# Kernel optimization log

Measured on AMD Instinct MI355X. Metric: run time of the kernel, lower is better.

## Reference

```python
import jax, jax.numpy as jnp
import numpy as np

B, S, E, D = 8, 2048, 1024, 512

def setup_inputs() -> dict:
    key = jax.random.key(0)
    ks = jax.random.split(key, 7)
    scale = 1.0 / np.sqrt(E)
    return {
        "X": jax.random.normal(ks[0], (B, S, E), dtype=jnp.float32),
        "lam": jnp.float32(0.8),
        "W_q": jax.random.uniform(ks[1], (E, 2 * D), jnp.float32, -scale, scale),
        "b_q": jax.random.uniform(ks[2], (2 * D,), jnp.float32, -scale, scale),
        "W_k": jax.random.uniform(ks[3], (E, 2 * D), jnp.float32, -scale, scale),
        "b_k": jax.random.uniform(ks[4], (2 * D,), jnp.float32, -scale, scale),
        "W_v": jax.random.uniform(ks[5], (E, D), jnp.float32, -scale, scale),
        "b_v": jax.random.uniform(ks[6], (D,), jnp.float32, -scale, scale),
    }

def reference(X, lam, W_q, b_q, W_k, b_k, W_v, b_v):
    # Projections
    Q = X @ W_q + b_q          # [B, S, 2D]
    K = X @ W_k + b_k          # [B, S, 2D]
    V = X @ W_v + b_v          # [B, S, D]
    Q1, Q2 = Q[..., :D], Q[..., D:]
    K1, K2 = K[..., :D], K[..., D:]
    s = 1.0 / np.sqrt(D)
    A1 = jnp.einsum('bqd,bkd->bqk', Q1, K1) * s  # [B, S, S]
    A2 = jnp.einsum('bqd,bkd->bqk', Q2, K2) * s
    P = jax.nn.softmax(A1, axis=-1) - lam * jax.nn.softmax(A2, axis=-1)
    return jnp.einsum('bqk,bkd->bqd', P, V)      # [B, S, D]
```

## Files before the change

### kernel.cpp

```cpp
#include <hip/hip_runtime.h>


typedef unsigned short u16;
typedef short    bf16x8 __attribute__((ext_vector_type(8)));
typedef unsigned short u16x8 __attribute__((ext_vector_type(8)));
typedef unsigned short u16x4 __attribute__((ext_vector_type(4)));
typedef float    f32x4  __attribute__((ext_vector_type(4)));

typedef __attribute__((address_space(3))) unsigned int       lds_uint;
typedef __attribute__((address_space(1))) const unsigned int gl_uint;

__device__ __forceinline__ void glds16(const void* g, void* l) {
  __builtin_amdgcn_global_load_lds((gl_uint*)g, (lds_uint*)l, 16, 0, 0);
}

__device__ __forceinline__ u16 to_bf16(float f) {
  unsigned u = __float_as_uint(f);
  return (u16)((u + 0x7FFFu + ((u >> 16) & 1u)) >> 16);
}
__device__ __forceinline__ float b2f(u16 h) {
  return __uint_as_float(((unsigned)h) << 16);
}


__global__ void cvt_x(const float4* __restrict__ in, u16x4* __restrict__ out, int n4) {
  int i = blockIdx.x * 256 + threadIdx.x;
  if (i >= n4) return;
  float4 v = in[i];
  u16x4 o;
  o[0] = to_bf16(v.x); o[1] = to_bf16(v.y); o[2] = to_bf16(v.z); o[3] = to_bf16(v.w);
  out[i] = o;
}

__global__ void transpose_cvt(const float* __restrict__ in, u16* __restrict__ out,
                              int R, int C) {
  __shared__ float t[64][65];
  int c0 = blockIdx.x * 64, r0 = blockIdx.y * 64;
  int tx = threadIdx.x, ty = threadIdx.y;
  #pragma unroll
  for (int i = 0; i < 64; i += 4)
    t[ty + i][tx] = in[(long)(r0 + ty + i) * C + c0 + tx];
  __syncthreads();
  #pragma unroll
  for (int i = 0; i < 64; i += 4)
    out[(long)(c0 + ty + i) * R + r0 + tx] = to_bf16(t[tx][ty + i]);
}

__global__ void concat2(const float* __restrict__ a, const float* __restrict__ b,
                        float* __restrict__ o, int n) {
  int i = blockIdx.x * 256 + threadIdx.x;
  if (i < n) o[i] = a[i];
  else if (i < 2 * n) o[i] = b[i - n];
}

__device__ __forceinline__ void swizzle_tiles(int& tm, int& tn) {
  int nx = gridDim.x;
  int lin = blockIdx.y * nx + blockIdx.x;
  int span = nx * 4;
  int group = lin / span;
  int ing = lin % span;
  tm = group * 4 + (ing & 3);
  tn = ing >> 2;
}

__global__ __launch_bounds__(256, 4) void gemm_nt(
    const u16* __restrict__ A, int lda,
    const u16* __restrict__ B, int ldb,
    u16* __restrict__ C1, u16* __restrict__ C2, int splitN, int ldc,
    int Kd, float scale,
    const float* __restrict__ bias, int biasMode)
{
  __shared__ u16 SM[2][8192];
  u16* As = SM[0];
  u16* Bs = SM[1];

  int tid = threadIdx.x;
  int wave = tid >> 6, lane = tid & 63;
  int quad = lane >> 4, ln = lane & 15;
  int wm = wave >> 1, wn = wave & 1;
  int tm, tn;
  swizzle_tiles(tm, tn);
  int c8 = lane >> 3, ml = lane & 7;

  const f32x4 fz = {0.f, 0.f, 0.f, 0.f};
  f32x4 acc[4][4];
  #pragma unroll
  for (int i = 0; i < 4; i++)
    #pragma unroll
    for (int j = 0; j < 4; j++) acc[i][j] = fz;

  const u16* Abase = A + (long)(tm * 128 + ml) * lda + c8 * 8;
  const u16* Bbase = B + (long)(tn * 128 + ml) * ldb + c8 * 8;

  for (int kt = 0; kt < Kd; kt += 64) {
    __syncthreads();
    #pragma unroll
    for (int i = 0; i < 4; i++) {
      int mg = wave * 4 + i;
      glds16(Abase + (long)mg * 8 * lda + kt, &As[mg * 512]);
      glds16(Bbase + (long)mg * 8 * ldb + kt, &Bs[mg * 512]);
    }
    __syncthreads();
    #pragma unroll
    for (int ks = 0; ks < 2; ks++) {
      bf16x8 af[4], bfr[4];
      int c = ks * 4 + quad;
      #pragma unroll
      for (int mt = 0; mt < 4; mt++) {
        int m = wm * 64 + mt * 16 + ln;
        af[mt] = *(const bf16x8*)&As[((m >> 3) * 64 + c * 8 + (m & 7)) * 8];
      }
      #pragma unroll
      for (int nt = 0; nt < 4; nt++) {
        int n = wn * 64 + nt * 16 + ln;
        bfr[nt] = *(const bf16x8*)&Bs[((n >> 3) * 64 + c * 8 + (n & 7)) * 8];
      }
      #pragma unroll
      for (int mt = 0; mt < 4; mt++)
        #pragma unroll
        for (int nt = 0; nt < 4; nt++)
          acc[mt][nt] = __builtin_amdgcn_mfma_f32_16x16x32_bf16(af[mt], bfr[nt], acc[mt][nt], 0, 0, 0);
    }
  }

  int rowBase = tm * 128 + wm * 64;
  int colBase = tn * 128 + wn * 64;
  u16* Cw = C1; int outCol = colBase;
  if (colBase >= splitN) { Cw = C2; outCol = colBase - splitN; }
  u16* eb = &SM[0][0] + wave * 4096;

  __syncthreads();
  #pragma unroll
  for (int mt = 0; mt < 4; mt++) {
    #pragma unroll
    for (int nt = 0; nt < 4; nt++) {
      int colL = nt * 16 + ln;
      float bcol = (biasMode == 1) ? bias[colBase + colL] : 0.f;
      #pragma unroll
      for (int r = 0; r < 4; r++) {
        int rowL = mt * 16 + quad * 4 + r;
        float brow = (biasMode == 2) ? bias[rowBase + rowL] : 0.f;
        float v = acc[mt][nt][r] * scale + bcol + brow;
        eb[rowL * 64 + (((colL >> 3) ^ (rowL & 7)) << 3) + (colL & 7)] = to_bf16(v);
      }
    }
  }
  {
    int row = lane;
    long gr = (long)(rowBase + row) * ldc + outCol;
    #pragma unroll
    for (int c = 0; c < 8; c++) {
      u16x8 ch = *(const u16x8*)&eb[row * 64 + ((c ^ (row & 7)) << 3)];
      *(u16x8*)&Cw[gr + c * 8] = ch;
    }
  }
}

__device__ __forceinline__ void gemm256_core(
    const u16* __restrict__ A, int lda,
    const u16* __restrict__ B, int ldb,
    int NT, int tm, int tn, u16* SMp, f32x4 (&acc)[8][4])
{
  int tid = threadIdx.x;
  int wave = tid >> 6, lane = tid & 63;
  int quad = lane >> 4, ln = lane & 15;
  int wm = wave >> 2, wn = wave & 3;
  int c8 = lane >> 3, ml = lane & 7;

  const f32x4 fz = {0.f, 0.f, 0.f, 0.f};
  #pragma unroll
  for (int i = 0; i < 8; i++)
    #pragma unroll
    for (int j = 0; j < 4; j++) acc[i][j] = fz;

  const u16* Ab = A + (long)(tm * 256 + ml) * lda + c8 * 8;
  const u16* Bb = B + (long)(tn * 256 + ml) * ldb + c8 * 8;

  #pragma unroll
  for (int h = 0; h < 2; h++) {
    int hg = h * 16 + wave * 2;
    glds16(Ab + (long)(hg * 8) * lda,       SMp + hg * 512);
    glds16(Ab + (long)(hg * 8 + 8) * lda,   SMp + (hg + 1) * 512);
  }
  #pragma unroll
  for (int h = 0; h < 2; h++) {
    int hg = h * 16 + wave * 2;
    glds16(Bb + (long)(hg * 8) * ldb,       SMp + 2 * 16384 + hg * 512);
    glds16(Bb + (long)(hg * 8 + 8) * ldb,   SMp + 2 * 16384 + (hg + 1) * 512);
  }
  {
    int kt1 = (NT > 1) ? 64 : 0;
    #pragma unroll
    for (int h = 0; h < 2; h++) {
      int hg = h * 16 + wave * 2;
      glds16(Bb + (long)(hg * 8) * ldb + kt1,     SMp + 3 * 16384 + hg * 512);
      glds16(Bb + (long)(hg * 8 + 8) * ldb + kt1, SMp + 3 * 16384 + (hg + 1) * 512);
    }
  }
  asm volatile("s_waitcnt vmcnt(4)" ::: "memory");
  __builtin_amdgcn_s_barrier();
  __builtin_amdgcn_sched_barrier(0);

  for (int t = 0; t < NT; t++) {
    const int p = t & 1;
    const u16* Ar = SMp + p * 16384;
    const u16* Br = SMp + (2 + p) * 16384;
    bf16x8 bfr[2][4];

    #pragma unroll
    for (int q = 0; q < 4; q++) {
      bf16x8 af[2][2];
      #pragma unroll
      for (int dm = 0; dm < 2; dm++) {
        int m = wm * 128 + (q * 2 + dm) * 16 + ln;
        #pragma unroll
        for (int ks = 0; ks < 2; ks++)
          af[dm][ks] = *(const bf16x8*)(Ar + ((m >> 3) * 64 + (ks * 4 + quad) * 8 + (m & 7)) * 8);
      }
      if (q == 0) {
        #pragma unroll
        for (int nt = 0; nt < 4; nt++) {
          int n = wn * 64 + nt * 16 + ln;
          #pragma unroll
          for (int ks = 0; ks < 2; ks++)
            bfr[ks][nt] = *(const bf16x8*)(Br + ((n >> 3) * 64 + (ks * 4 + quad) * 8 + (n & 7)) * 8);
        }
      }
      if (q < 2) {
        int ktA = ((t + 1 < NT) ? (t + 1) : (NT - 1)) << 6;
        int hg = q * 16 + wave * 2;
        u16* dst = SMp + ((t + 1) & 1) * 16384;
        glds16(Ab + (long)(hg * 8) * lda + ktA,     dst + hg * 512);
        glds16(Ab + (long)(hg * 8 + 8) * lda + ktA, dst + (hg + 1) * 512);
      } else {
        int ktB = ((t + 2 < NT) ? (t + 2) : (NT - 1)) << 6;
        int hg = (q - 2) * 16 + wave * 2;
        u16* dst = SMp + (2 + p) * 16384;
        glds16(Bb + (long)(hg * 8) * ldb + ktB,     dst + hg * 512);
        glds16(Bb + (long)(hg * 8 + 8) * ldb + ktB, dst + (hg + 1) * 512);
      }
      __builtin_amdgcn_sched_barrier(0);
      __builtin_amdgcn_s_barrier();
      asm volatile("s_waitcnt lgkmcnt(0)" ::: "memory");
      __builtin_amdgcn_sched_barrier(0);
      __builtin_amdgcn_s_setprio(1);
      #pragma unroll
      for (int ks = 0; ks < 2; ks++)
        #pragma unroll
        for (int dm = 0; dm < 2; dm++)
          #pragma unroll
          for (int nt = 0; nt < 4; nt++)
            acc[q * 2 + dm][nt] = __builtin_amdgcn_mfma_f32_16x16x32_bf16(
                af[dm][ks], bfr[ks][nt], acc[q * 2 + dm][nt], 0, 0, 0);
      __builtin_amdgcn_s_setprio(0);
      __builtin_amdgcn_sched_barrier(0);
      if (q == 3) asm volatile("s_waitcnt vmcnt(4)" ::: "memory");
      __builtin_amdgcn_s_barrier();
      __builtin_amdgcn_sched_barrier(0);
    }
  }
}

__global__ __launch_bounds__(512, 2) void gemm_nt256(
    const u16* __restrict__ A, int lda,
    const u16* __restrict__ B, int ldb,
    u16* __restrict__ C1, u16* __restrict__ C2, int splitN, int ldc,
    int Kd, float scale,
    const float* __restrict__ bias, int biasMode)
{
  __shared__ u16 SM[4][16384];
  int tm, tn;
  swizzle_tiles(tm, tn);
  f32x4 acc[8][4];
  gemm256_core(A, lda, B, ldb, Kd >> 6, tm, tn, &SM[0][0], acc);

  int tid = threadIdx.x;
  int wave = tid >> 6, lane = tid & 63;
  int quad = lane >> 4, ln = lane & 15;
  int wm = wave >> 2, wn = wave & 3;

  int rowBase = tm * 256 + wm * 128;
  int colBase = tn * 256 + wn * 64;
  u16* Cw = C1; int outCol = colBase;
  if (colBase >= splitN) { Cw = C2; outCol = colBase - splitN; }
  u16* eb = &SM[0][0] + wave * 8192;

  asm volatile("s_waitcnt vmcnt(0)" ::: "memory");
  __builtin_amdgcn_s_barrier();
  __builtin_amdgcn_sched_barrier(0);

  #pragma unroll
  for (int mt = 0; mt < 8; mt++) {
    #pragma unroll
    for (int nt = 0; nt < 4; nt++) {
      int colL = nt * 16 + ln;
      float bcol = (biasMode == 1) ? bias[colBase + colL] : 0.f;
      #pragma unroll
      for (int r = 0; r < 4; r++) {
        int rowL = mt * 16 + quad * 4 + r;
        float brow = (biasMode == 2) ? bias[rowBase + rowL] : 0.f;
        float v = acc[mt][nt][r] * scale + bcol + brow;
        eb[rowL * 64 + (((colL >> 3) ^ (rowL & 7)) << 3) + (colL & 7)] = to_bf16(v);
      }
    }
  }
  #pragma unroll
  for (int rr = 0; rr < 2; rr++) {
    int row = rr * 64 + lane;
    long gr = (long)(rowBase + row) * ldc + outCol;
    #pragma unroll
    for (int c = 0; c < 8; c++) {
      u16x8 ch = *(const u16x8*)&eb[row * 64 + ((c ^ (row & 7)) << 3)];
      *(u16x8*)&Cw[gr + c * 8] = ch;
    }
  }
}

__global__ __launch_bounds__(512, 2) void gemm_s256(
    const u16* __restrict__ Q, const u16* __restrict__ K,
    u16* __restrict__ E1, u16* __restrict__ E2,
    float* __restrict__ statsP, float scale)
{
  __shared__ u16 SM[4][16384];
  int bz = blockIdx.z >> 1, half = blockIdx.z & 1;
  const u16* A = Q + (long)bz * 2097152 + half * 512;
  const u16* B = K + (long)bz * 2097152 + half * 512;
  u16* Ed = (half ? E2 : E1) + (long)bz * 4194304;
  statsP += (long)blockIdx.z * 65536;

  int tm, tn;
  swizzle_tiles(tm, tn);
  f32x4 acc[8][4];
  gemm256_core(A, 1024, B, 1024, 8 , tm, tn, &SM[0][0], acc);

  int tid = threadIdx.x;
  int wave = tid >> 6, lane = tid & 63;
  int quad = lane >> 4, ln = lane & 15;
  int wm = wave >> 2, wn = wave & 3;

  int rowBase = tm * 256 + wm * 128;
  int colBase = tn * 256 + wn * 64;
  int kb = tn * 4 + wn;
  u16* eb = &SM[0][0] + wave * 8192;

  asm volatile("s_waitcnt vmcnt(0)" ::: "memory");
  __builtin_amdgcn_s_barrier();
  __builtin_amdgcn_sched_barrier(0);

  #pragma unroll
  for (int mt = 0; mt < 8; mt++) {
    #pragma unroll
    for (int nt = 0; nt < 4; nt++) {
      int colL = nt * 16 + ln;
      #pragma unroll
      for (int r = 0; r < 4; r++) {
        int rowL = mt * 16 + quad * 4 + r;
        eb[rowL * 64 + (((colL >> 3) ^ (rowL & 7)) << 3) + (colL & 7)] =
            to_bf16(__expf(acc[mt][nt][r] * scale));
      }
    }
  }
  #pragma unroll
  for (int rr = 0; rr < 2; rr++) {
    int row = rr * 64 + lane;
    u16x8 ch[8];
    #pragma unroll
    for (int c = 0; c < 8; c++)
      ch[c] = *(const u16x8*)&eb[row * 64 + ((c ^ (row & 7)) << 3)];
    u16* Ep = Ed + (long)(rowBase + row) * 2048 + colBase;
    #pragma unroll
    for (int c = 0; c < 8; c++)
      *(u16x8*)&Ep[c * 8] = ch[c];
    float L = 0.f;
    #pragma unroll
    for (int c = 0; c < 8; c++)
      #pragma unroll
      for (int j = 0; j < 8; j++) L += b2f(ch[c][j]);
    statsP[(rowBase + row) * 32 + kb] = L;
  }
}

__global__ void stats_reduce(const float* __restrict__ sp, float* __restrict__ so,
                             const float* __restrict__ lamPtr) {
  int gid = blockIdx.x * 256 + threadIdx.x;
  const float* p = sp + (long)gid * 32;
  float L = 0.f;
  #pragma unroll
  for (int kb = 0; kb < 32; kb++) L += p[kb];
  int half = (gid >> 11) & 1;
  so[gid] = (half ? lamPtr[0] : 1.0f) / L;
}

__global__ __launch_bounds__(512, 2) void apply_pv(
    const u16* __restrict__ E1, const u16* __restrict__ E2,
    const u16* __restrict__ VT, const float* __restrict__ inv,
    float* __restrict__ Out)
{
  __shared__ u16 Vs[2][32768];
  __shared__ u16 Pb[2][4096];
  __shared__ float i1s[64], i2s[64];

  const int NT = 32;
  int b = blockIdx.x & 7, qt = blockIdx.x >> 3;
  int q0 = qt * 64;
  int tid = threadIdx.x;
  int wave = tid >> 6, lane = tid & 63, quad = lane >> 4, ln = lane & 15;
  int c8 = lane >> 3, ml = lane & 7;
  int r = tid >> 3, cg8 = tid & 7;

  const u16* e1p = E1 + ((long)b * 2048 + q0 + r) * 2048 + cg8 * 8;
  const u16* e2p = E2 + ((long)b * 2048 + q0 + r) * 2048 + cg8 * 8;
  const u16* Vbase = VT + (long)b * 2048;
  int pw = (r >> 3) * 512 + cg8 * 64 + (r & 7) * 8;

  const f32x4 fz = {0.f, 0.f, 0.f, 0.f};
  f32x4 acc[4][4];
  #pragma unroll
  for (int i = 0; i < 4; i++)
    #pragma unroll
    for (int j = 0; j < 4; j++) acc[i][j] = fz;

  if (tid < 64)       i1s[tid]       = inv[(long)(b * 2 + 0) * 2048 + q0 + tid];
  else if (tid < 128) i2s[tid - 64]  = inv[(long)(b * 2 + 1) * 2048 + q0 + (tid - 64)];
  u16x8 a1 = *(const u16x8*)(e1p);
  u16x8 a2 = *(const u16x8*)(e2p);
  __builtin_amdgcn_sched_barrier(0);
  #pragma unroll
  for (int i = 0; i < 8; i++) {
    int dg = wave * 8 + i;
    glds16(Vbase + (long)(dg * 8 + ml) * 16384 + c8 * 8, &Vs[0][dg * 512]);
  }
  __builtin_amdgcn_sched_barrier(0);
  asm volatile("s_waitcnt lgkmcnt(0)" ::: "memory");
  __builtin_amdgcn_s_barrier();
  __builtin_amdgcn_sched_barrier(0);
  float i1 = i1s[r], i2 = i2s[r];
  {
    u16x8 o;
    #pragma unroll
    for (int j = 0; j < 8; j++)
      o[j] = to_bf16(b2f(a1[j]) * i1 - b2f(a2[j]) * i2);
    *(u16x8*)&Pb[0][pw] = o;
  }
  a1 = *(const u16x8*)(e1p + 64);
  a2 = *(const u16x8*)(e2p + 64);
  __builtin_amdgcn_sched_barrier(0);
  asm volatile("s_waitcnt lgkmcnt(0)" ::: "memory");
  asm volatile("s_waitcnt vmcnt(2)" ::: "memory");
  __builtin_amdgcn_sched_barrier(0);
  __builtin_amdgcn_s_barrier();
  __builtin_amdgcn_sched_barrier(0);

  for (int t = 0; t < NT; t++) {
    const int p = t & 1;
    const u16* Vr = &Vs[p][0];
    const u16* Pr = &Pb[p][0];
    u16* Vw = &Vs[p ^ 1][0];
    u16* Pw = &Pb[p ^ 1][0];
    int ktv = ((t + 1 < NT) ? (t + 1) : (NT - 1)) << 6;
    int kte = ((t + 2 < NT) ? (t + 2) : (NT - 1)) << 6;
    bf16x8 vf[2][4];

    #pragma unroll
    for (int q = 0; q < 4; q++) {
      bf16x8 pf[2];
      #pragma unroll
      for (int ks = 0; ks < 2; ks++) {
        int m = q * 16 + ln;
        pf[ks] = *(const bf16x8*)&Pr[((m >> 3) * 64 + (ks * 4 + quad) * 8 + (m & 7)) * 8];
      }
      if (q == 0) {
        #pragma unroll
        for (int ks = 0; ks < 2; ks++)
          #pragma unroll
          for (int nt = 0; nt < 4; nt++) {
            int d = wave * 64 + nt * 16 + ln;
            vf[ks][nt] = *(const bf16x8*)&Vr[((d >> 3) * 64 + (ks * 4 + quad) * 8 + (d & 7)) * 8];
          }
      }
      #pragma unroll
      for (int i = 0; i < 2; i++) {
        int dg = wave * 8 + q * 2 + i;
        glds16(Vbase + (long)(dg * 8 + ml) * 16384 + ktv + c8 * 8, Vw + dg * 512);
      }
      if (q == 3) {
        __builtin_amdgcn_sched_barrier(0);
        u16x8 o;
        #pragma unroll
        for (int j = 0; j < 8; j++)
          o[j] = to_bf16(b2f(a1[j]) * i1 - b2f(a2[j]) * i2);
        *(u16x8*)&Pw[pw] = o;
        a1 = *(const u16x8*)(e1p + kte);
        a2 = *(const u16x8*)(e2p + kte);
      }
      __builtin_amdgcn_sched_barrier(0);
      __builtin_amdgcn_s_barrier();
      asm volatile("s_waitcnt lgkmcnt(0)" ::: "memory");
      __builtin_amdgcn_sched_barrier(0);
      __builtin_amdgcn_s_setprio(1);
      #pragma unroll
      for (int ks = 0; ks < 2; ks++)
        #pragma unroll
        for (int nt = 0; nt < 4; nt++)
          acc[q][nt] = __builtin_amdgcn_mfma_f32_16x16x32_bf16(pf[ks], vf[ks][nt], acc[q][nt], 0, 0, 0);
      __builtin_amdgcn_s_setprio(0);
      __builtin_amdgcn_sched_barrier(0);
      if (q == 3) asm volatile("s_waitcnt vmcnt(2)" ::: "memory");
      __builtin_amdgcn_s_barrier();
      __builtin_amdgcn_sched_barrier(0);
    }
  }

  #pragma unroll
  for (int mt = 0; mt < 4; mt++)
    #pragma unroll
    for (int nt = 0; nt < 4; nt++)
      #pragma unroll
      for (int r2 = 0; r2 < 4; r2++)
        Out[((long)b * 2048 + q0 + mt * 16 + quad * 4 + r2) * 512 + wave * 64 + nt * 16 + ln] =
            acc[mt][nt][r2];
}


extern "C" void kernel_launch(void* const* d_in, const int* in_sizes, int n_in,
                              void* d_out, int out_size, void* d_ws, size_t ws_size,
                              hipStream_t stream)
{
  const float* X   = (const float*)d_in[0];
  const float* lam = (const float*)d_in[1];
  const float* Wq  = (const float*)d_in[2];
  const float* bq  = (const float*)d_in[3];
  const float* Wk  = (const float*)d_in[4];
  const float* bk  = (const float*)d_in[5];
  const float* Wv  = (const float*)d_in[6];
  const float* bv  = (const float*)d_in[7];
  float* Out = (float*)d_out;
  char* ws = (char*)d_ws;

  u16*  WqkT   = (u16*)(ws + 0);
  u16*  WvT    = (u16*)(ws + 4194304);
  float* bqk   = (float*)(ws + 5242880);
  u16*  Qb     = (u16*)(ws + 6291456);
  u16*  Kb     = (u16*)(ws + 39845888);
  u16*  VTb    = (u16*)(ws + 73400320);
  u16*  Xb     = (u16*)(ws + 90177536);
  u16*  E1     = (u16*)(ws + 90177536);
  u16*  E2     = (u16*)(ws + 157286400);
  float* statsP= (float*)(ws + 224395264);
  float* invD  = (float*)(ws + 228589568);

  cvt_x<<<16384, 256, 0, stream>>>((const float4*)X, (u16x4*)Xb, 4194304);
  transpose_cvt<<<dim3(16, 16), dim3(64, 4), 0, stream>>>(Wq, WqkT, 1024, 1024);
  transpose_cvt<<<dim3(16, 16), dim3(64, 4), 0, stream>>>(Wk, WqkT + 1024 * 1024, 1024, 1024);
  transpose_cvt<<<dim3(8, 16),  dim3(64, 4), 0, stream>>>(Wv, WvT, 1024, 512);
  concat2<<<8, 256, 0, stream>>>(bq, bk, bqk, 1024);

  gemm_nt256<<<dim3(8, 64), 512, 0, stream>>>(Xb, 1024, WqkT, 1024,
                                              Qb, Kb, 1024, 1024,
                                              1024, 1.0f, bqk, 1);
  gemm_nt<<<dim3(128, 4), 256, 0, stream>>>(WvT, 1024, Xb, 1024,
                                            VTb, VTb, 1 << 30, 16384,
                                            1024, 1.0f, bv, 2);

  const float s = 0.044194173824159216f;
  gemm_s256<<<dim3(8, 8, 16), 512, 0, stream>>>(Qb, Kb, E1, E2, statsP, s);

  stats_reduce<<<128, 256, 0, stream>>>(statsP, invD, lam);
  apply_pv<<<256, 512, 0, stream>>>(E1, E2, VTb, invD, Out);
}
```

Before: 475.6 us.

## Triple-buffer B tiles and drop per-subtile barriers in GEMM main loop

The shared GEMM core now uses three LDS buffers for the B operand instead of two. At the top of each k-iteration it issues all global-to-LDS loads for the next A tile and the B tile two steps ahead. It then runs the full MFMA block with a single wait and barrier per iteration, replacing the four barrier/lgkmcnt/setprio sections per iteration. The aim is to cut synchronisation overhead and let the compiler schedule LDS reads freely. The cost is LDS per block rising from 128KB to 160KB, and fewer points where prefetch traffic is interleaved with compute.

```diff
diff --git a/kernel.cpp b/kernel.cpp
--- a/kernel.cpp
+++ b/kernel.cpp
@@ -185,79 +185,81 @@
   #pragma unroll
   for (int h = 0; h < 2; h++) {
     int hg = h * 16 + wave * 2;
-    glds16(Bb + (long)(hg * 8) * ldb,       SMp + 2 * 16384 + hg * 512);
-    glds16(Bb + (long)(hg * 8 + 8) * ldb,   SMp + 2 * 16384 + (hg + 1) * 512);
+    glds16(Bb + (long)(hg * 8) * ldb,       SMp + 32768 + hg * 512);
+    glds16(Bb + (long)(hg * 8 + 8) * ldb,   SMp + 32768 + (hg + 1) * 512);
   }
   {
     int kt1 = (NT > 1) ? 64 : 0;
     #pragma unroll
     for (int h = 0; h < 2; h++) {
       int hg = h * 16 + wave * 2;
-      glds16(Bb + (long)(hg * 8) * ldb + kt1,     SMp + 3 * 16384 + hg * 512);
-      glds16(Bb + (long)(hg * 8 + 8) * ldb + kt1, SMp + 3 * 16384 + (hg + 1) * 512);
+      glds16(Bb + (long)(hg * 8) * ldb + kt1,     SMp + 49152 + hg * 512);
+      glds16(Bb + (long)(hg * 8 + 8) * ldb + kt1, SMp + 49152 + (hg + 1) * 512);
     }
   }
   asm volatile("s_waitcnt vmcnt(4)" ::: "memory");
   __builtin_amdgcn_s_barrier();
   __builtin_amdgcn_sched_barrier(0);
 
+  int bcur = 0;
   for (int t = 0; t < NT; t++) {
     const int p = t & 1;
     const u16* Ar = SMp + p * 16384;
-    const u16* Br = SMp + (2 + p) * 16384;
+    const u16* Br = SMp + 32768 + bcur * 16384;
+
+    {
+      int ktA = ((t + 1 < NT) ? (t + 1) : (NT - 1)) << 6;
+      u16* dA = SMp + ((t + 1) & 1) * 16384;
+      #pragma unroll
+      for (int h = 0; h < 2; h++) {
+        int hg = h * 16 + wave * 2;
+        glds16(Ab + (long)(hg * 8) * lda + ktA,     dA + hg * 512);
+        glds16(Ab + (long)(hg * 8 + 8) * lda + ktA, dA + (hg + 1) * 512);
+      }
+      int ktB = ((t + 2 < NT) ? (t + 2) : (NT - 1)) << 6;
+      int bst = bcur + 2; if (bst >= 3) bst -= 3;
+      u16* dB = SMp + 32768 + bst * 16384;
+      #pragma unroll
+      for (int h = 0; h < 2; h++) {
+        int hg = h * 16 + wave * 2;
+        glds16(Bb + (long)(hg * 8) * ldb + ktB,     dB + hg * 512);
+        glds16(Bb + (long)(hg * 8 + 8) * ldb + ktB, dB + (hg + 1) * 512);
+      }
+    }
+    __builtin_amdgcn_sched_barrier(0);
+
     bf16x8 bfr[2][4];
-
-    #pragma unroll
-    for (int q = 0; q < 4; q++) {
+    #pragma unroll
+    for (int nt = 0; nt < 4; nt++) {
+      int n = wn * 64 + nt * 16 + ln;
+      #pragma unroll
+      for (int ks = 0; ks < 2; ks++)
+        bfr[ks][nt] = *(const bf16x8*)(Br + ((n >> 3) * 64 + (ks * 4 + quad) * 8 + (n & 7)) * 8);
+    }
+    #pragma unroll
+    for (int g = 0; g < 4; g++) {
       bf16x8 af[2][2];
       #pragma unroll
       for (int dm = 0; dm < 2; dm++) {
-        int m = wm * 128 + (q * 2 + dm) * 16 + ln;
+        int m = wm * 128 + (g * 2 + dm) * 16 + ln;
         #pragma unroll
         for (int ks = 0; ks < 2; ks++)
           af[dm][ks] = *(const bf16x8*)(Ar + ((m >> 3) * 64 + (ks * 4 + quad) * 8 + (m & 7)) * 8);
       }
-      if (q == 0) {
-        #pragma unroll
-        for (int nt = 0; nt < 4; nt++) {
-          int n = wn * 64 + nt * 16 + ln;
-          #pragma unroll
-          for (int ks = 0; ks < 2; ks++)
-            bfr[ks][nt] = *(const bf16x8*)(Br + ((n >> 3) * 64 + (ks * 4 + quad) * 8 + (n & 7)) * 8);
-        }
-      }
-      if (q < 2) {
-        int ktA = ((t + 1 < NT) ? (t + 1) : (NT - 1)) << 6;
-        int hg = q * 16 + wave * 2;
-        u16* dst = SMp + ((t + 1) & 1) * 16384;
-        glds16(Ab + (long)(hg * 8) * lda + ktA,     dst + hg * 512);
-        glds16(Ab + (long)(hg * 8 + 8) * lda + ktA, dst + (hg + 1) * 512);
-      } else {
-        int ktB = ((t + 2 < NT) ? (t + 2) : (NT - 1)) << 6;
-        int hg = (q - 2) * 16 + wave * 2;
-        u16* dst = SMp + (2 + p) * 16384;
-        glds16(Bb + (long)(hg * 8) * ldb + ktB,     dst + hg * 512);
-        glds16(Bb + (long)(hg * 8 + 8) * ldb + ktB, dst + (hg + 1) * 512);
-      }
-      __builtin_amdgcn_sched_barrier(0);
-      __builtin_amdgcn_s_barrier();
-      asm volatile("s_waitcnt lgkmcnt(0)" ::: "memory");
-      __builtin_amdgcn_sched_barrier(0);
-      __builtin_amdgcn_s_setprio(1);
       #pragma unroll
       for (int ks = 0; ks < 2; ks++)
         #pragma unroll
         for (int dm = 0; dm < 2; dm++)
           #pragma unroll
           for (int nt = 0; nt < 4; nt++)
-            acc[q * 2 + dm][nt] = __builtin_amdgcn_mfma_f32_16x16x32_bf16(
-                af[dm][ks], bfr[ks][nt], acc[q * 2 + dm][nt], 0, 0, 0);
-      __builtin_amdgcn_s_setprio(0);
-      __builtin_amdgcn_sched_barrier(0);
-      if (q == 3) asm volatile("s_waitcnt vmcnt(4)" ::: "memory");
-      __builtin_amdgcn_s_barrier();
-      __builtin_amdgcn_sched_barrier(0);
-    }
+            acc[g * 2 + dm][nt] = __builtin_amdgcn_mfma_f32_16x16x32_bf16(
+                af[dm][ks], bfr[ks][nt], acc[g * 2 + dm][nt], 0, 0, 0);
+    }
+
+    asm volatile("s_waitcnt vmcnt(4)" ::: "memory");
+    __builtin_amdgcn_s_barrier();
+    __builtin_amdgcn_sched_barrier(0);
+    bcur = (bcur == 2) ? 0 : bcur + 1;
   }
 }
 
@@ -268,7 +270,7 @@
     int Kd, float scale,
     const float* __restrict__ bias, int biasMode)
 {
-  __shared__ u16 SM[4][16384];
+  __shared__ u16 SM[5][16384];
   int tm, tn;
   swizzle_tiles(tm, tn);
   f32x4 acc[8][4];
@@ -321,7 +323,7 @@
     u16* __restrict__ E1, u16* __restrict__ E2,
     float* __restrict__ statsP, float scale)
 {
-  __shared__ u16 SM[4][16384];
+  __shared__ u16 SM[5][16384];
   int bz = blockIdx.z >> 1, half = blockIdx.z & 1;
   const u16* A = Q + (long)bz * 2097152 + half * 512;
   const u16* B = K + (long)bz * 2097152 + half * 512;
```

After: 478.9 us. No clear change (+0.7%).

## Make QK projection and score GEMMs persistent with multi-tile continuous pipelines

Applied to the files above, without the earlier changes.

Replaces the one-tile-per-block 256x256 GEMMs with persistent 256-block kernels. Each block walks several M tiles back to back (two for the projection, four for the score GEMM) in a single continuous K-loop pipeline, and runs the epilogue inline every 16 or 8 K-steps through a small per-wave LDS staging buffer. The goal is to remove per-tile prologue and epilogue pipeline drain, keep the B tile's locality across the M tiles, and fit the grid to the CU count. In exchange, epilogue stores and exp/stat work now stall the MFMA pipeline mid-loop, and LDS usage rises to 160 KB per block.

```diff
diff --git a/kernel.cpp b/kernel.cpp
--- a/kernel.cpp
+++ b/kernel.cpp
@@ -156,55 +156,71 @@
   }
 }
 
-__device__ __forceinline__ void gemm256_core(
-    const u16* __restrict__ A, int lda,
-    const u16* __restrict__ B, int ldb,
-    int NT, int tm, int tn, u16* SMp, f32x4 (&acc)[8][4])
+
+__global__ __launch_bounds__(512, 2) void gemm_s256p(
+    const u16* __restrict__ Q, const u16* __restrict__ K,
+    u16* __restrict__ E1, u16* __restrict__ E2,
+    float* __restrict__ statsP, float scale)
 {
+  __shared__ u16 SM[81920];
+
+  int blk = blockIdx.x;
+  int g = blk & 7, s2 = blk >> 3;
+  int p_ = g + 8 * (s2 >> 3);
+  int tn = s2 & 7;
+  int tmg = p_ & 1;
+  int z = p_ >> 1;
+  int bz = z >> 1, half = z & 1;
+
+  const u16* A = Q + (long)bz * 2097152 + half * 512;
+  const u16* B = K + (long)bz * 2097152 + half * 512;
+  u16* Ed = (half ? E2 : E1) + (long)bz * 4194304;
+  float* sp = statsP + (long)z * 65536;
+
   int tid = threadIdx.x;
-  int wave = tid >> 6, lane = tid & 63;
-  int quad = lane >> 4, ln = lane & 15;
+  int wave = tid >> 6, lane = tid & 63, quad = lane >> 4, ln = lane & 15;
   int wm = wave >> 2, wn = wave & 3;
   int c8 = lane >> 3, ml = lane & 7;
 
   const f32x4 fz = {0.f, 0.f, 0.f, 0.f};
+  f32x4 acc[8][4];
   #pragma unroll
   for (int i = 0; i < 8; i++)
     #pragma unroll
     for (int j = 0; j < 4; j++) acc[i][j] = fz;
 
-  const u16* Ab = A + (long)(tm * 256 + ml) * lda + c8 * 8;
-  const u16* Bb = B + (long)(tn * 256 + ml) * ldb + c8 * 8;
+  const u16* Abase = A + (long)(tmg * 1024 + ml) * 1024 + c8 * 8;
+  const u16* Bbase = B + (long)(tn * 256 + ml) * 1024 + c8 * 8;
+  u16* eb = SM + 65536 + wave * 2048;
+  const int NTT = 32;
 
   #pragma unroll
   for (int h = 0; h < 2; h++) {
     int hg = h * 16 + wave * 2;
-    glds16(Ab + (long)(hg * 8) * lda,       SMp + hg * 512);
-    glds16(Ab + (long)(hg * 8 + 8) * lda,   SMp + (hg + 1) * 512);
+    glds16(Abase + (long)(hg * 8) * 1024,       SM + hg * 512);
+    glds16(Abase + (long)(hg * 8 + 8) * 1024,   SM + (hg + 1) * 512);
   }
   #pragma unroll
   for (int h = 0; h < 2; h++) {
     int hg = h * 16 + wave * 2;
-    glds16(Bb + (long)(hg * 8) * ldb,       SMp + 2 * 16384 + hg * 512);
-    glds16(Bb + (long)(hg * 8 + 8) * ldb,   SMp + 2 * 16384 + (hg + 1) * 512);
-  }
-  {
-    int kt1 = (NT > 1) ? 64 : 0;
-    #pragma unroll
-    for (int h = 0; h < 2; h++) {
-      int hg = h * 16 + wave * 2;
-      glds16(Bb + (long)(hg * 8) * ldb + kt1,     SMp + 3 * 16384 + hg * 512);
-      glds16(Bb + (long)(hg * 8 + 8) * ldb + kt1, SMp + 3 * 16384 + (hg + 1) * 512);
-    }
+    glds16(Bbase + (long)(hg * 8) * 1024,       SM + 32768 + hg * 512);
+    glds16(Bbase + (long)(hg * 8 + 8) * 1024,   SM + 32768 + (hg + 1) * 512);
+  }
+  #pragma unroll
+  for (int h = 0; h < 2; h++) {
+    int hg = h * 16 + wave * 2;
+    glds16(Bbase + (long)(hg * 8) * 1024 + 64,     SM + 49152 + hg * 512);
+    glds16(Bbase + (long)(hg * 8 + 8) * 1024 + 64, SM + 49152 + (hg + 1) * 512);
   }
   asm volatile("s_waitcnt vmcnt(4)" ::: "memory");
   __builtin_amdgcn_s_barrier();
   __builtin_amdgcn_sched_barrier(0);
 
-  for (int t = 0; t < NT; t++) {
-    const int p = t & 1;
-    const u16* Ar = SMp + p * 16384;
-    const u16* Br = SMp + (2 + p) * 16384;
+  for (int T = 0; T < NTT; T++) {
+    const u16* Ar = SM + (T & 1) * 16384;
+    const u16* Br = SM + 32768 + (T & 1) * 16384;
+    int Ta = (T + 1 < NTT) ? T + 1 : NTT - 1;
+    int Tb = (T + 2 < NTT) ? T + 2 : NTT - 1;
     bf16x8 bfr[2][4];
 
     #pragma unroll
@@ -227,17 +243,17 @@
         }
       }
       if (q < 2) {
-        int ktA = ((t + 1 < NT) ? (t + 1) : (NT - 1)) << 6;
         int hg = q * 16 + wave * 2;
-        u16* dst = SMp + ((t + 1) & 1) * 16384;
-        glds16(Ab + (long)(hg * 8) * lda + ktA,     dst + hg * 512);
-        glds16(Ab + (long)(hg * 8 + 8) * lda + ktA, dst + (hg + 1) * 512);
+        u16* dst = SM + (Ta & 1) * 16384;
+        long ao = (long)((Ta >> 3) * 256 + hg * 8) * 1024 + ((Ta & 7) << 6);
+        glds16(Abase + ao,            dst + hg * 512);
+        glds16(Abase + ao + 8 * 1024, dst + (hg + 1) * 512);
       } else {
-        int ktB = ((t + 2 < NT) ? (t + 2) : (NT - 1)) << 6;
         int hg = (q - 2) * 16 + wave * 2;
-        u16* dst = SMp + (2 + p) * 16384;
-        glds16(Bb + (long)(hg * 8) * ldb + ktB,     dst + hg * 512);
-        glds16(Bb + (long)(hg * 8 + 8) * ldb + ktB, dst + (hg + 1) * 512);
+        u16* dst = SM + 32768 + (Tb & 1) * 16384;
+        long bo = (long)(hg * 8) * 1024 + ((Tb & 7) << 6);
+        glds16(Bbase + bo,            dst + hg * 512);
+        glds16(Bbase + bo + 8 * 1024, dst + (hg + 1) * 512);
       }
       __builtin_amdgcn_sched_barrier(0);
       __builtin_amdgcn_s_barrier();
@@ -258,126 +274,210 @@
       __builtin_amdgcn_s_barrier();
       __builtin_amdgcn_sched_barrier(0);
     }
-  }
-}
-
-__global__ __launch_bounds__(512, 2) void gemm_nt256(
-    const u16* __restrict__ A, int lda,
-    const u16* __restrict__ B, int ldb,
+
+    if ((T & 7) == 7) {
+      int sub = T >> 3;
+      int rowBase0 = (tmg * 4 + sub) * 256 + wm * 128;
+      int colBase = tn * 256 + wn * 64;
+      int kb = tn * 4 + wn;
+      #pragma unroll
+      for (int c2 = 0; c2 < 4; c2++) {
+        #pragma unroll
+        for (int gg = 0; gg < 2; gg++) {
+          #pragma unroll
+          for (int nt = 0; nt < 4; nt++) {
+            int colL = nt * 16 + ln;
+            #pragma unroll
+            for (int r = 0; r < 4; r++) {
+              int rowL = gg * 16 + quad * 4 + r;
+              eb[rowL * 64 + (((colL >> 3) ^ (rowL & 7)) << 3) + (colL & 7)] =
+                  to_bf16(__expf(acc[c2 * 2 + gg][nt][r] * scale));
+            }
+          }
+        }
+        {
+          int row = lane & 31, hf = lane >> 5;
+          float L = 0.f;
+          u16x8 ch[4];
+          #pragma unroll
+          for (int cc = 0; cc < 4; cc++) {
+            int c = hf * 4 + cc;
+            ch[cc] = *(const u16x8*)&eb[row * 64 + ((c ^ (row & 7)) << 3)];
+            #pragma unroll
+            for (int j = 0; j < 8; j++) L += b2f(ch[cc][j]);
+          }
+          u16* Ep = Ed + (long)(rowBase0 + c2 * 32 + row) * 2048 + colBase + hf * 32;
+          #pragma unroll
+          for (int cc = 0; cc < 4; cc++)
+            *(u16x8*)&Ep[cc * 8] = ch[cc];
+          L += __shfl_xor(L, 32);
+          if (hf == 0)
+            sp[(rowBase0 + c2 * 32 + row) * 32 + kb] = L;
+        }
+      }
+      #pragma unroll
+      for (int i = 0; i < 8; i++)
+        #pragma unroll
+        for (int j = 0; j < 4; j++) acc[i][j] = fz;
+    }
+  }
+  asm volatile("s_waitcnt vmcnt(0)" ::: "memory");
+}
+
+__global__ __launch_bounds__(512, 2) void gemm_nt256p(
+    const u16* __restrict__ A, const u16* __restrict__ B,
     u16* __restrict__ C1, u16* __restrict__ C2, int splitN, int ldc,
-    int Kd, float scale,
-    const float* __restrict__ bias, int biasMode)
+    float scale, const float* __restrict__ bias, int biasMode)
 {
-  __shared__ u16 SM[4][16384];
-  int tm, tn;
-  swizzle_tiles(tm, tn);
+  __shared__ u16 SM[81920];
+
+  int blk = blockIdx.x;
+  int g = blk & 7, s2 = blk >> 3;
+  int tmg = g + 8 * (s2 >> 3);
+  int tn = s2 & 7;
+
+  int tid = threadIdx.x;
+  int wave = tid >> 6, lane = tid & 63, quad = lane >> 4, ln = lane & 15;
+  int wm = wave >> 2, wn = wave & 3;
+  int c8 = lane >> 3, ml = lane & 7;
+
+  const f32x4 fz = {0.f, 0.f, 0.f, 0.f};
   f32x4 acc[8][4];
-  gemm256_core(A, lda, B, ldb, Kd >> 6, tm, tn, &SM[0][0], acc);
-
-  int tid = threadIdx.x;
-  int wave = tid >> 6, lane = tid & 63;
-  int quad = lane >> 4, ln = lane & 15;
-  int wm = wave >> 2, wn = wave & 3;
-
-  int rowBase = tm * 256 + wm * 128;
-  int colBase = tn * 256 + wn * 64;
-  u16* Cw = C1; int outCol = colBase;
-  if (colBase >= splitN) { Cw = C2; outCol = colBase - splitN; }
-  u16* eb = &SM[0][0] + wave * 8192;
-
+  #pragma unroll
+  for (int i = 0; i < 8; i++)
+    #pragma unroll
+    for (int j = 0; j < 4; j++) acc[i][j] = fz;
+
+  const u16* Abase = A + (long)(tmg * 512 + ml) * 1024 + c8 * 8;
+  const u16* Bbase = B + (long)(tn * 256 + ml) * 1024 + c8 * 8;
+  u16* eb = SM + 65536 + wave * 2048;
+  const int NTT = 32;
+
+  #pragma unroll
+  for (int h = 0; h < 2; h++) {
+    int hg = h * 16 + wave * 2;
+    glds16(Abase + (long)(hg * 8) * 1024,       SM + hg * 512);
+    glds16(Abase + (long)(hg * 8 + 8) * 1024,   SM + (hg + 1) * 512);
+  }
+  #pragma unroll
+  for (int h = 0; h < 2; h++) {
+    int hg = h * 16 + wave * 2;
+    glds16(Bbase + (long)(hg * 8) * 1024,       SM + 32768 + hg * 512);
+    glds16(Bbase + (long)(hg * 8 + 8) * 1024,   SM + 32768 + (hg + 1) * 512);
+  }
+  #pragma unroll
+  for (int h = 0; h < 2; h++) {
+    int hg = h * 16 + wave * 2;
+    glds16(Bbase + (long)(hg * 8) * 1024 + 64,     SM + 49152 + hg * 512);
+    glds16(Bbase + (long)(hg * 8 + 8) * 1024 + 64, SM + 49152 + (hg + 1) * 512);
+  }
+  asm volatile("s_waitcnt vmcnt(4)" ::: "memory");
+  __builtin_amdgcn_s_barrier();
+  __builtin_amdgcn_sched_barrier(0);
+
+  for (int T = 0; T < NTT; T++) {
+    const u16* Ar = SM + (T & 1) * 16384;
+    const u16* Br = SM + 32768 + (T & 1) * 16384;
+    int Ta = (T + 1 < NTT) ? T + 1 : NTT - 1;
+    int Tb = (T + 2 < NTT) ? T + 2 : NTT - 1;
+    bf16x8 bfr[2][4];
+
+    #pragma unroll
+    for (int q = 0; q < 4; q++) {
+      bf16x8 af[2][2];
+      #pragma unroll
+      for (int dm = 0; dm < 2; dm++) {
+        int m = wm * 128 + (q * 2 + dm) * 16 + ln;
+        #pragma unroll
+        for (int ks = 0; ks < 2; ks++)
+          af[dm][ks] = *(const bf16x8*)(Ar + ((m >> 3) * 64 + (ks * 4 + quad) * 8 + (m & 7)) * 8);
+      }
+      if (q == 0) {
+        #pragma unroll
+        for (int nt = 0; nt < 4; nt++) {
+          int n = wn * 64 + nt * 16 + ln;
+          #pragma unroll
+          for (int ks = 0; ks < 2; ks++)
+            bfr[ks][nt] = *(const bf16x8*)(Br + ((n >> 3) * 64 + (ks * 4 + quad) * 8 + (n & 7)) * 8);
+        }
+      }
+      if (q < 2) {
+        int hg = q * 16 + wave * 2;
+        u16* dst = SM + (Ta & 1) * 16384;
+        long ao = (long)((Ta >> 4) * 256 + hg * 8) * 1024 + ((Ta & 15) << 6);
+        glds16(Abase + ao,            dst + hg * 512);
+        glds16(Abase + ao + 8 * 1024, dst + (hg + 1) * 512);
+      } else {
+        int hg = (q - 2) * 16 + wave * 2;
+        u16* dst = SM + 32768 + (Tb & 1) * 16384;
+        long bo = (long)(hg * 8) * 1024 + ((Tb & 15) << 6);
+        glds16(Bbase + bo,            dst + hg * 512);
+        glds16(Bbase + bo + 8 * 1024, dst + (hg + 1) * 512);
+      }
+      __builtin_amdgcn_sched_barrier(0);
+      __builtin_amdgcn_s_barrier();
+      asm volatile("s_waitcnt lgkmcnt(0)" ::: "memory");
+      __builtin_amdgcn_sched_barrier(0);
+      __builtin_amdgcn_s_setprio(1);
+      #pragma unroll
+      for (int ks = 0; ks < 2; ks++)
+        #pragma unroll
+        for (int dm = 0; dm < 2; dm++)
+          #pragma unroll
+          for (int nt = 0; nt < 4; nt++)
+            acc[q * 2 + dm][nt] = __builtin_amdgcn_mfma_f32_16x16x32_bf16(
+                af[dm][ks], bfr[ks][nt], acc[q * 2 + dm][nt], 0, 0, 0);
+      __builtin_amdgcn_s_setprio(0);
+      __builtin_amdgcn_sched_barrier(0);
+      if (q == 3) asm volatile("s_waitcnt vmcnt(4)" ::: "memory");
+      __builtin_amdgcn_s_barrier();
+      __builtin_amdgcn_sched_barrier(0);
+    }
+
+    if ((T & 15) == 15) {
+      int sub = T >> 4;
+      int rowBase0 = (tmg * 2 + sub) * 256 + wm * 128;
+      int colBase = tn * 256 + wn * 64;
+      u16* Cw = C1; int outCol = colBase;
+      if (colBase >= splitN) { Cw = C2; outCol = colBase - splitN; }
+      #pragma unroll
+      for (int c2 = 0; c2 < 4; c2++) {
+        #pragma unroll
+        for (int gg = 0; gg < 2; gg++) {
+          #pragma unroll
+          for (int nt = 0; nt < 4; nt++) {
+            int colL = nt * 16 + ln;
+            float bcol = (biasMode == 1) ? bias[colBase + colL] : 0.f;
+            #pragma unroll
+            for (int r = 0; r < 4; r++) {
+              int rowL = gg * 16 + quad * 4 + r;
+              float brow = (biasMode == 2) ? bias[rowBase0 + c2 * 32 + rowL] : 0.f;
+              float v = acc[c2 * 2 + gg][nt][r] * scale + bcol + brow;
+              eb[rowL * 64 + (((colL >> 3) ^ (rowL & 7)) << 3) + (colL & 7)] = to_bf16(v);
+            }
+          }
+        }
+        {
+          int row = lane & 31, hf = lane >> 5;
+          u16x8 ch[4];
+          #pragma unroll
+          for (int cc = 0; cc < 4; cc++) {
+            int c = hf * 4 + cc;
+            ch[cc] = *(const u16x8*)&eb[row * 64 + ((c ^ (row & 7)) << 3)];
+          }
+          long gr = (long)(rowBase0 + c2 * 32 + row) * ldc + outCol + hf * 32;
+          #pragma unroll
+          for (int cc = 0; cc < 4; cc++)
+            *(u16x8*)&Cw[gr + cc * 8] = ch[cc];
+        }
+      }
+      #pragma unroll
+      for (int i = 0; i < 8; i++)
+        #pragma unroll
+        for (int j = 0; j < 4; j++) acc[i][j] = fz;
+    }
+  }
   asm volatile("s_waitcnt vmcnt(0)" ::: "memory");
-  __builtin_amdgcn_s_barrier();
-  __builtin_amdgcn_sched_barrier(0);
-
-  #pragma unroll
-  for (int mt = 0; mt < 8; mt++) {
-    #pragma unroll
-    for (int nt = 0; nt < 4; nt++) {
-      int colL = nt * 16 + ln;
-      float bcol = (biasMode == 1) ? bias[colBase + colL] : 0.f;
-      #pragma unroll
-      for (int r = 0; r < 4; r++) {
-        int rowL = mt * 16 + quad * 4 + r;
-        float brow = (biasMode == 2) ? bias[rowBase + rowL] : 0.f;
-        float v = acc[mt][nt][r] * scale + bcol + brow;
-        eb[rowL * 64 + (((colL >> 3) ^ (rowL & 7)) << 3) + (colL & 7)] = to_bf16(v);
-      }
-    }
-  }
-  #pragma unroll
-  for (int rr = 0; rr < 2; rr++) {
-    int row = rr * 64 + lane;
-    long gr = (long)(rowBase + row) * ldc + outCol;
-    #pragma unroll
-    for (int c = 0; c < 8; c++) {
-      u16x8 ch = *(const u16x8*)&eb[row * 64 + ((c ^ (row & 7)) << 3)];
-      *(u16x8*)&Cw[gr + c * 8] = ch;
-    }
-  }
-}
-
-__global__ __launch_bounds__(512, 2) void gemm_s256(
-    const u16* __restrict__ Q, const u16* __restrict__ K,
-    u16* __restrict__ E1, u16* __restrict__ E2,
-    float* __restrict__ statsP, float scale)
-{
-  __shared__ u16 SM[4][16384];
-  int bz = blockIdx.z >> 1, half = blockIdx.z & 1;
-  const u16* A = Q + (long)bz * 2097152 + half * 512;
-  const u16* B = K + (long)bz * 2097152 + half * 512;
-  u16* Ed = (half ? E2 : E1) + (long)bz * 4194304;
-  statsP += (long)blockIdx.z * 65536;
-
-  int tm, tn;
-  swizzle_tiles(tm, tn);
-  f32x4 acc[8][4];
-  gemm256_core(A, 1024, B, 1024, 8 , tm, tn, &SM[0][0], acc);
-
-  int tid = threadIdx.x;
-  int wave = tid >> 6, lane = tid & 63;
-  int quad = lane >> 4, ln = lane & 15;
-  int wm = wave >> 2, wn = wave & 3;
-
-  int rowBase = tm * 256 + wm * 128;
-  int colBase = tn * 256 + wn * 64;
-  int kb = tn * 4 + wn;
-  u16* eb = &SM[0][0] + wave * 8192;
-
-  asm volatile("s_waitcnt vmcnt(0)" ::: "memory");
-  __builtin_amdgcn_s_barrier();
-  __builtin_amdgcn_sched_barrier(0);
-
-  #pragma unroll
-  for (int mt = 0; mt < 8; mt++) {
-    #pragma unroll
-    for (int nt = 0; nt < 4; nt++) {
-      int colL = nt * 16 + ln;
-      #pragma unroll
-      for (int r = 0; r < 4; r++) {
-        int rowL = mt * 16 + quad * 4 + r;
-        eb[rowL * 64 + (((colL >> 3) ^ (rowL & 7)) << 3) + (colL & 7)] =
-            to_bf16(__expf(acc[mt][nt][r] * scale));
-      }
-    }
-  }
-  #pragma unroll
-  for (int rr = 0; rr < 2; rr++) {
-    int row = rr * 64 + lane;
-    u16x8 ch[8];
-    #pragma unroll
-    for (int c = 0; c < 8; c++)
-      ch[c] = *(const u16x8*)&eb[row * 64 + ((c ^ (row & 7)) << 3)];
-    u16* Ep = Ed + (long)(rowBase + row) * 2048 + colBase;
-    #pragma unroll
-    for (int c = 0; c < 8; c++)
-      *(u16x8*)&Ep[c * 8] = ch[c];
-    float L = 0.f;
-    #pragma unroll
-    for (int c = 0; c < 8; c++)
-      #pragma unroll
-      for (int j = 0; j < 8; j++) L += b2f(ch[c][j]);
-    statsP[(rowBase + row) * 32 + kb] = L;
-  }
 }
 
 __global__ void stats_reduce(const float* __restrict__ sp, float* __restrict__ so,
@@ -555,15 +655,14 @@
   transpose_cvt<<<dim3(8, 16),  dim3(64, 4), 0, stream>>>(Wv, WvT, 1024, 512);
   concat2<<<8, 256, 0, stream>>>(bq, bk, bqk, 1024);
 
-  gemm_nt256<<<dim3(8, 64), 512, 0, stream>>>(Xb, 1024, WqkT, 1024,
-                                              Qb, Kb, 1024, 1024,
-                                              1024, 1.0f, bqk, 1);
+  gemm_nt256p<<<256, 512, 0, stream>>>(Xb, WqkT, Qb, Kb, 1024, 1024,
+                                       1.0f, bqk, 1);
   gemm_nt<<<dim3(128, 4), 256, 0, stream>>>(WvT, 1024, Xb, 1024,
                                             VTb, VTb, 1 << 30, 16384,
                                             1024, 1.0f, bv, 2);
 
   const float s = 0.044194173824159216f;
-  gemm_s256<<<dim3(8, 8, 16), 512, 0, stream>>>(Qb, Kb, E1, E2, statsP, s);
+  gemm_s256p<<<256, 512, 0, stream>>>(Qb, Kb, E1, E2, statsP, s);
 
   stats_reduce<<<128, 256, 0, stream>>>(statsP, invD, lam);
   apply_pv<<<256, 512, 0, stream>>>(E1, E2, VTb, invD, Out);
```

Result: faster. 461.0 us (-3.1%).
